# Performance work log

Measured on AMD Instinct MI355X. Metric: run time of the kernel, lower is better.

Reference implementation:

```python
import jax, jax.numpy as jnp
import numpy as np

B, N, D, L, H = 4, 256, 256, 256, 128
PAIR_DIM = 2 * D + 3 + L  # 771


def setup_inputs() -> dict:
    key = jax.random.key(0)
    ks = jax.random.split(key, 6)
    object_features = jax.random.normal(ks[0], (B, N, D), dtype=jnp.float32)
    language_embedding = jax.random.normal(ks[1], (B, L), dtype=jnp.float32)
    centers = jax.random.normal(ks[2], (B, N, 3), dtype=jnp.float32)
    object_mask = jax.random.randint(ks[3], (B, N), 0, 2).astype(bool)
    object_mask = object_mask.at[:, 0].set(True)  # ensure >=1 valid object per scene
    W1 = jax.random.normal(ks[4], (PAIR_DIM, H), dtype=jnp.float32) * (PAIR_DIM ** -0.5)
    b1 = jnp.zeros((H,), dtype=jnp.float32)
    W2 = jax.random.normal(ks[5], (H, 1), dtype=jnp.float32) * (H ** -0.5)
    b2 = jnp.zeros((1,), dtype=jnp.float32)
    return {"object_features": object_features, "language_embedding": language_embedding,
            "centers": centers, "object_mask": object_mask,
            "W1": W1, "b1": b1, "W2": W2, "b2": b2}


def reference(object_features, language_embedding, centers, object_mask, W1, b1, W2, b2):
    # Decompose the first Linear over the concatenated pair input
    # cat([feat_i, feat_j, rel_pos, lang]) @ W1 == feat_i@W1a + feat_j@W1b + rel@W1c + lang@W1d
    d = object_features.shape[-1]
    W1_i, W1_j = W1[:d], W1[d:2 * d]
    W1_rel, W1_lang = W1[2 * d:2 * d + 3], W1[2 * d + 3:]

    s_i = jnp.einsum('bnd,dh->bnh', object_features, W1_i)      # [B,N,H]
    s_j = jnp.einsum('bnd,dh->bnh', object_features, W1_j)      # [B,N,H]
    s_lang = jnp.einsum('bl,lh->bh', language_embedding, W1_lang)  # [B,H]

    rel = (centers[:, :, None, :] - centers[:, None, :, :]) / 5.0  # [B,N,N,3]
    s_rel = jnp.einsum('bnjc,ch->bnjh', rel, W1_rel)               # [B,N,N,H]

    hidden = jax.nn.relu(s_i[:, :, None, :] + s_j[:, None, :, :] + s_rel
                         + s_lang[:, None, None, :] + b1)          # [B,N,N,H]
    scores = jnp.einsum('bnjh,ho->bnj', hidden, W2) + b2[0]        # [B,N,N]

    pair_mask = object_mask[:, :, None] & object_mask[:, None, :]
    scores = jnp.where(pair_mask, scores, -1e9)

    relation_weights = jax.nn.softmax(scores, axis=2)
    relation_context = jnp.einsum('bnj,bjd->bnd', relation_weights, object_features)
    enhanced_features = object_features + relation_context  # use_residual=True
    return enhanced_features, relation_weights
```

## Files before the change

### kernel.cpp

```cpp
#include <hip/hip_runtime.h>

#define B_ 4
#define N_ 256
#define D_ 256
#define L_ 256
#define H_ 128
#define NB_ 4
#define G_  8
#define TPB_ 1024
#define GRID_ (B_ * N_ / NB_)
#define MAGIC_ 0x5F3759DFu
#define CH_ 16
#define NCH_ (H_ / CH_)

__global__ __launch_bounds__(TPB_) void prm_kernel(
    const float* __restrict__ feat,
    const float* __restrict__ lang,
    const float* __restrict__ centers,
    const float* __restrict__ W1,
    const float* __restrict__ b1,
    const float* __restrict__ W2,
    const float* __restrict__ b2,
    const unsigned char* __restrict__ mraw,
    float* __restrict__ Bt,
    unsigned int* __restrict__ sent,
    float* __restrict__ outEnh,
    float* __restrict__ outW)
{
    __shared__ __align__(16) float fs[NB_][D_];
    __shared__ __align__(16) float ls[L_];
    __shared__ float cs[NB_][3];
    __shared__ __align__(16) float As[NB_][H_];
    __shared__ __align__(16) float W2s[H_];
    __shared__ unsigned char msk[N_];
    __shared__ int layoutByte;
    __shared__ __align__(16) union {
        float red[G_][2 * NB_ + 1][H_];
        struct {
            float part[4][NB_][N_];
            float wsh[NB_][N_];
            float sbt[2][CH_][N_];
        } p2;
    } u;

    const int tiles = N_ / NB_;
    const int b  = blockIdx.x / tiles;
    const int n0 = (blockIdx.x % tiles) * NB_;
    const int t  = threadIdx.x;

    if (t == 0) layoutByte = 0;
    if (t < 256) {
        uchar4 v = ((const uchar4*)mraw)[t];
        if (v.y | v.z | v.w) layoutByte = 1;
    }

    {
        int r = t >> 8, d = t & (D_ - 1);
        fs[r][d] = feat[((b * N_) + (n0 + r)) * D_ + d];
    }
    if (t < L_) ls[t] = lang[b * L_ + t];
    if (t < NB_ * 3) {
        int r = t / 3, c = t % 3;
        cs[r][c] = centers[((b * N_) + (n0 + r)) * 3 + c] * 0.2f;
    }
    __syncthreads();

    if (t < N_) {
        msk[t] = layoutByte ? (mraw[b * N_ + t] != 0)
                            : (((const int*)mraw)[b * N_ + t] != 0);
    }
    if (t >= 512 && t < 512 + H_) W2s[t - 512] = W2[t - 512];

    {
        const int g = t >> 7;
        const int h = t & (H_ - 1);
        float si[NB_] = {0.f, 0.f, 0.f, 0.f};
        float sj[NB_] = {0.f, 0.f, 0.f, 0.f};
        float sl = 0.f;
        const float* __restrict__ Wi = W1 + h;
        const float* __restrict__ Wj = W1 + D_ * H_ + h;
        const float* __restrict__ Wl = W1 + (2 * D_ + 3) * H_ + h;

        const int d0 = g * (D_ / G_);
        for (int dd = d0; dd < d0 + D_ / G_; dd += 4) {
            float wi[4], wj[4], wl[4];
#pragma unroll
            for (int k = 0; k < 4; ++k) {
                wi[k] = Wi[(dd + k) * H_];
                wj[k] = Wj[(dd + k) * H_];
                wl[k] = Wl[(dd + k) * H_];
            }
            const float4 lv = *(const float4*)&ls[dd];
            sl += lv.x * wl[0] + lv.y * wl[1] + lv.z * wl[2] + lv.w * wl[3];
#pragma unroll
            for (int r = 0; r < NB_; ++r) {
                const float4 fv = *(const float4*)&fs[r][dd];
                si[r] += fv.x * wi[0] + fv.y * wi[1] + fv.z * wi[2] + fv.w * wi[3];
                sj[r] += fv.x * wj[0] + fv.y * wj[1] + fv.z * wj[2] + fv.w * wj[3];
            }
        }

#pragma unroll
        for (int r = 0; r < NB_; ++r) {
            u.red[g][r][h]       = si[r];
            u.red[g][NB_ + r][h] = sj[r];
        }
        u.red[g][2 * NB_][h] = sl;
    }
    __syncthreads();

    if (t < H_) {
        float sit[NB_] = {0.f, 0.f, 0.f, 0.f};
        float sjt[NB_] = {0.f, 0.f, 0.f, 0.f};
        float slt = 0.f;
#pragma unroll
        for (int gg = 0; gg < G_; ++gg) {
#pragma unroll
            for (int r = 0; r < NB_; ++r) {
                sit[r] += u.red[gg][r][t];
                sjt[r] += u.red[gg][NB_ + r][t];
            }
            slt += u.red[gg][2 * NB_][t];
        }
        const float wr0 = W1[(2 * D_ + 0) * H_ + t];
        const float wr1 = W1[(2 * D_ + 1) * H_ + t];
        const float wr2 = W1[(2 * D_ + 2) * H_ + t];
        const float bb  = b1[t];
        float bv[NB_];
        float* btp = &Bt[((size_t)(b * H_) + t) * N_ + n0];
#pragma unroll
        for (int r = 0; r < NB_; ++r) {
            float srel = cs[r][0] * wr0 + cs[r][1] * wr1 + cs[r][2] * wr2;
            As[r][t] = sit[r] + srel;
            bv[r]    = sjt[r] - srel + slt + bb;
        }
        asm volatile("global_store_dword %4, %0, off sc0 sc1\n\t"
                     "global_store_dword %4, %1, off offset:4 sc0 sc1\n\t"
                     "global_store_dword %4, %2, off offset:8 sc0 sc1\n\t"
                     "global_store_dword %4, %3, off offset:12 sc0 sc1"
                     :: "v"(bv[0]), "v"(bv[1]), "v"(bv[2]), "v"(bv[3]),
                        "v"(btp)
                     : "memory");
        asm volatile("s_waitcnt vmcnt(0)" ::: "memory");
    }
    __syncthreads();
    if (t == 0)
        __hip_atomic_store(&sent[blockIdx.x], MAGIC_, __ATOMIC_RELAXED,
                           __HIP_MEMORY_SCOPE_AGENT);

    if (t < 64) {
        const unsigned int* sp = &sent[b * 64 + t];
        while (!__all(__hip_atomic_load(sp, __ATOMIC_RELAXED,
                                        __HIP_MEMORY_SCOPE_AGENT) == MAGIC_)) {
            __builtin_amdgcn_s_sleep(1);
        }
    }
    __syncthreads();

    const int q = t >> 8;
    const int j = t & (N_ - 1);
    const int w = t >> 6;
    const int l = t & 63;

    {
        const float* cb = Bt + (size_t)(b * H_) * N_;
        float acc[NB_] = {0.f, 0.f, 0.f, 0.f};
        float4 v;
        {
            const float* a0 = cb + (0 * CH_ + w) * N_ + l * 4;
            asm volatile("global_load_dwordx4 %0, %1, off sc0 sc1"
                         : "=v"(v) : "v"(a0));
        }
        for (int c = 0; c < NCH_; ++c) {
            asm volatile("s_waitcnt vmcnt(0)" ::: "memory");
            __builtin_amdgcn_sched_barrier(0);
            *(float4*)&u.p2.sbt[c & 1][w][l * 4] = v;
            __syncthreads();
            if (c + 1 < NCH_) {
                const float* a1 = cb + ((c + 1) * CH_ + w) * N_ + l * 4;
                asm volatile("global_load_dwordx4 %0, %1, off sc0 sc1"
                             : "=v"(v) : "v"(a1));
            }
#pragma unroll
            for (int k = 0; k < 4; ++k) {
                const int hl = q * 4 + k;
                const int h  = c * CH_ + hl;
                const float bt = u.p2.sbt[c & 1][hl][j];
                const float w2 = W2s[h];
#pragma unroll
                for (int r = 0; r < NB_; ++r)
                    acc[r] += fmaxf(As[r][h] + bt, 0.f) * w2;
            }
        }
#pragma unroll
        for (int r = 0; r < NB_; ++r) u.p2.part[q][r][j] = acc[r];
    }
    __syncthreads();

    {
        const int wid = t >> 6, lane = t & 63;
        const float b2v = b2[0];
        if (wid < NB_) {
            const int r = wid;
            float sc[4], mx = -1e30f;
#pragma unroll
            for (int k = 0; k < 4; ++k) {
                int jj = lane + k * 64;
                float s = u.p2.part[0][r][jj] + u.p2.part[1][r][jj] +
                          u.p2.part[2][r][jj] + u.p2.part[3][r][jj] + b2v;
                if (!(msk[n0 + r] && msk[jj])) s = -1e9f;
                sc[k] = s;
                mx = fmaxf(mx, s);
            }
            for (int off = 32; off >= 1; off >>= 1)
                mx = fmaxf(mx, __shfl_xor(mx, off));
            float e[4], sm = 0.f;
#pragma unroll
            for (int k = 0; k < 4; ++k) { e[k] = __expf(sc[k] - mx); sm += e[k]; }
            for (int off = 32; off >= 1; off >>= 1) sm += __shfl_xor(sm, off);
            const float inv = 1.f / sm;
#pragma unroll
            for (int k = 0; k < 4; ++k) {
                int jj = lane + k * 64;
                float wgt = e[k] * inv;
                u.p2.wsh[r][jj] = wgt;
                outW[(((size_t)(b * N_) + (n0 + r)) * N_) + jj] = wgt;
            }
        }
    }
    __syncthreads();

    {
        const float* __restrict__ fb = feat + (size_t)b * N_ * D_;
        const int d = j;
        float facc[NB_] = {0.f, 0.f, 0.f, 0.f};
        for (int jj = q * 64; jj < q * 64 + 64; jj += 4) {
            float f0 = fb[(jj + 0) * D_ + d];
            float f1 = fb[(jj + 1) * D_ + d];
            float f2 = fb[(jj + 2) * D_ + d];
            float f3 = fb[(jj + 3) * D_ + d];
#pragma unroll
            for (int r = 0; r < NB_; ++r) {
                const float4 wv = *(const float4*)&u.p2.wsh[r][jj];
                facc[r] += wv.x * f0 + wv.y * f1 + wv.z * f2 + wv.w * f3;
            }
        }
        __syncthreads();
#pragma unroll
        for (int r = 0; r < NB_; ++r) u.p2.part[q][r][d] = facc[r];
    }
    __syncthreads();

    if (t < N_) {
        const float* __restrict__ fb = feat + (size_t)b * N_ * D_;
        const int d = t;
#pragma unroll
        for (int r = 0; r < NB_; ++r) {
            float v2 = u.p2.part[0][r][d] + u.p2.part[1][r][d] +
                       u.p2.part[2][r][d] + u.p2.part[3][r][d] +
                       fb[(n0 + r) * D_ + d];
            outEnh[((b * N_) + (n0 + r)) * D_ + d] = v2;
        }
    }
}

extern "C" void kernel_launch(void* const* d_in, const int* in_sizes, int n_in,
                              void* d_out, int out_size, void* d_ws, size_t ws_size,
                              hipStream_t stream) {
    const float* feat    = (const float*)d_in[0];
    const float* lang    = (const float*)d_in[1];
    const float* centers = (const float*)d_in[2];
    const unsigned char* mraw = (const unsigned char*)d_in[3];
    const float* W1      = (const float*)d_in[4];
    const float* b1      = (const float*)d_in[5];
    const float* W2      = (const float*)d_in[6];
    const float* b2      = (const float*)d_in[7];

    float* outEnh = (float*)d_out;
    float* outW   = (float*)d_out + (size_t)B_ * N_ * D_;

    float* Bt = (float*)d_ws;
    unsigned int* sent = (unsigned int*)((char*)d_ws +
                         (size_t)B_ * H_ * N_ * sizeof(float));

    prm_kernel<<<GRID_, TPB_, 0, stream>>>(feat, lang, centers, W1, b1, W2, b2,
                                           mraw, Bt, sent, outEnh, outW);
}
```

Before: 24.69 us.

## Deepen Bt prefetch pipeline with larger chunks and vectorized LDS reads

Doubles the hidden-dim chunk size, so each warp loads two rows per chunk. Two chunks of global loads are now kept in flight, and the four-chunk loop is fully unrolled with partial vmcnt waits. This halves the number of barriers and overlaps more load latency with compute. The inner loop now reads As and W2 as float4 and processes four hidden units per step, cutting scalar LDS reads. In exchange the double-buffered LDS staging area doubles in size and register pressure rises, which may affect occupancy.

Result: slower. 25.23 us (+2.2%).

```diff
diff --git a/kernel.cpp b/kernel.cpp
--- a/kernel.cpp
+++ b/kernel.cpp
@@ -10,7 +10,7 @@
 #define TPB_ 1024
 #define GRID_ (B_ * N_ / NB_)
 #define MAGIC_ 0x5F3759DFu
-#define CH_ 16
+#define CH_ 32
 #define NCH_ (H_ / CH_)
 
 __global__ __launch_bounds__(TPB_) void prm_kernel(
@@ -164,34 +164,57 @@
 
     {
         const float* cb = Bt + (size_t)(b * H_) * N_;
+        const float* base0 = cb + (w * 2 + 0) * N_ + l * 4;
+        const float* base1 = cb + (w * 2 + 1) * N_ + l * 4;
         float acc[NB_] = {0.f, 0.f, 0.f, 0.f};
-        float4 v;
-        {
-            const float* a0 = cb + (0 * CH_ + w) * N_ + l * 4;
-            asm volatile("global_load_dwordx4 %0, %1, off sc0 sc1"
-                         : "=v"(v) : "v"(a0));
-        }
-        for (int c = 0; c < NCH_; ++c) {
-            asm volatile("s_waitcnt vmcnt(0)" ::: "memory");
-            __builtin_amdgcn_sched_barrier(0);
-            *(float4*)&u.p2.sbt[c & 1][w][l * 4] = v;
-            __syncthreads();
-            if (c + 1 < NCH_) {
-                const float* a1 = cb + ((c + 1) * CH_ + w) * N_ + l * 4;
-                asm volatile("global_load_dwordx4 %0, %1, off sc0 sc1"
-                             : "=v"(v) : "v"(a1));
-            }
-#pragma unroll
-            for (int k = 0; k < 4; ++k) {
-                const int hl = q * 4 + k;
-                const int h  = c * CH_ + hl;
-                const float bt = u.p2.sbt[c & 1][hl][j];
-                const float w2 = W2s[h];
-#pragma unroll
-                for (int r = 0; r < NB_; ++r)
-                    acc[r] += fmaxf(As[r][h] + bt, 0.f) * w2;
-            }
-        }
+        float4 va0, va1, vb0, vb1;
+
+#define ISSUE1_(VREG, ADDR) \
+        asm volatile("global_load_dwordx4 %0, %1, off sc0 sc1" \
+                     : "=&v"(VREG) : "v"(ADDR))
+#define ISSUE_(V0, V1, c) do { \
+        ISSUE1_(V0, base0 + (c) * CH_ * N_); \
+        ISSUE1_(V1, base1 + (c) * CH_ * N_); } while (0)
+#define WAIT2_() do { asm volatile("s_waitcnt vmcnt(2)" ::: "memory"); \
+        __builtin_amdgcn_sched_barrier(0); } while (0)
+#define WAIT0_() do { asm volatile("s_waitcnt vmcnt(0)" ::: "memory"); \
+        __builtin_amdgcn_sched_barrier(0); } while (0)
+#define WRITE_(BUF, V0, V1) do { \
+        *(float4*)&u.p2.sbt[BUF][w * 2 + 0][l * 4] = V0; \
+        *(float4*)&u.p2.sbt[BUF][w * 2 + 1][l * 4] = V1; } while (0)
+#define COMPUTE_(c, BUF) do { \
+        _Pragma("unroll") \
+        for (int k4 = 0; k4 < 2; ++k4) { \
+            const int hl = q * 8 + k4 * 4; \
+            const int h  = (c) * CH_ + hl; \
+            const float4 w2v = *(const float4*)&W2s[h]; \
+            const float bt0 = u.p2.sbt[BUF][hl + 0][j]; \
+            const float bt1 = u.p2.sbt[BUF][hl + 1][j]; \
+            const float bt2 = u.p2.sbt[BUF][hl + 2][j]; \
+            const float bt3 = u.p2.sbt[BUF][hl + 3][j]; \
+            _Pragma("unroll") \
+            for (int r = 0; r < NB_; ++r) { \
+                const float4 av = *(const float4*)&As[r][h]; \
+                acc[r] += fmaxf(av.x + bt0, 0.f) * w2v.x \
+                        + fmaxf(av.y + bt1, 0.f) * w2v.y \
+                        + fmaxf(av.z + bt2, 0.f) * w2v.z \
+                        + fmaxf(av.w + bt3, 0.f) * w2v.w; \
+            } \
+        } } while (0)
+
+        ISSUE_(va0, va1, 0);
+        ISSUE_(vb0, vb1, 1);
+        WAIT2_(); WRITE_(0, va0, va1); __syncthreads();
+        ISSUE_(va0, va1, 2);
+        COMPUTE_(0, 0);
+        WAIT2_(); WRITE_(1, vb0, vb1); __syncthreads();
+        ISSUE_(vb0, vb1, 3);
+        COMPUTE_(1, 1);
+        WAIT2_(); WRITE_(0, va0, va1); __syncthreads();
+        COMPUTE_(2, 0);
+        WAIT0_(); WRITE_(1, vb0, vb1); __syncthreads();
+        COMPUTE_(3, 1);
+
 #pragma unroll
         for (int r = 0; r < NB_; ++r) u.p2.part[q][r][j] = acc[r];
     }
```
